# Performance work log

Measured on AMD Instinct MI355X. Metric: run time of the kernel, lower is better.

## Reference

```python
import jax, jax.numpy as jnp
import numpy as np

DIM = 768
N_HEADS = 12
HEAD_DIM = DIM // N_HEADS
BATCH = 2
SEQ = 4096


def setup_inputs() -> dict:
    key = jax.random.key(0)
    ks = jax.random.split(key, 9)
    s = 1.0 / np.sqrt(DIM)
    return {
        "x": jax.random.normal(ks[0], (BATCH, SEQ, DIM), dtype=jnp.float32),
        "Wq": jax.random.normal(ks[1], (DIM, DIM), dtype=jnp.float32) * s,
        "bq": jax.random.normal(ks[2], (DIM,), dtype=jnp.float32) * s,
        "Wk": jax.random.normal(ks[3], (DIM, DIM), dtype=jnp.float32) * s,
        "bk": jax.random.normal(ks[4], (DIM,), dtype=jnp.float32) * s,
        "Wv": jax.random.normal(ks[5], (DIM, DIM), dtype=jnp.float32) * s,
        "bv": jax.random.normal(ks[6], (DIM,), dtype=jnp.float32) * s,
        "Wo": jax.random.normal(ks[7], (DIM, DIM), dtype=jnp.float32) * s,
        "bo": jax.random.normal(ks[8], (DIM,), dtype=jnp.float32) * s,
    }


def reference(x, Wq, bq, Wk, bk, Wv, bv, Wo, bo):
    B, S, D = x.shape
    scale = 1.0 / np.sqrt(HEAD_DIM).astype(np.float32)
    # projections: [B,S,D] -> [B,H,S,Hd]
    def split_heads(t):
        return t.reshape(B, S, N_HEADS, HEAD_DIM).transpose(0, 2, 1, 3)
    q = split_heads(x @ Wq + bq)
    k = split_heads(x @ Wk + bk)
    v = split_heads(x @ Wv + bv)
    # full score matrix [B,H,S,S] as in the original (memory-bound)
    scores = jnp.einsum("bhqd,bhkd->bhqk", q, k) * scale
    attn = jax.nn.softmax(scores, axis=-1)
    out = jnp.einsum("bhqk,bhkd->bhqd", attn, v)
    out = out.transpose(0, 2, 1, 3).reshape(B, S, D)
    return out @ Wo + bo
```

## Files before the change

kernel.cpp:

```cpp
#include <hip/hip_runtime.h>
#include <hip/hip_bf16.h>
#include <math.h>

#define D_MODEL 768
#define NH 12
#define HD 64
#define BATCH 2
#define SEQ 4096
#define NROWS (BATCH * SEQ)

#define QSCALE 0.18033688011112042f

typedef __attribute__((ext_vector_type(8))) short short8;
typedef __attribute__((ext_vector_type(4))) short short4v;
typedef __attribute__((ext_vector_type(4))) float f32x4;
typedef __attribute__((ext_vector_type(16))) float f32x16;

__device__ inline unsigned short f2bf(float f) {
    __hip_bfloat16 h = __float2bfloat16(f);
    return *reinterpret_cast<unsigned short*>(&h);
}

__device__ __forceinline__ void async_ld16(const unsigned short* g, unsigned short* l) {
    __builtin_amdgcn_global_load_lds(
        (const __attribute__((address_space(1))) void*)g,
        (__attribute__((address_space(3))) void*)l, 16, 0, 0);
}

__global__ __launch_bounds__(256) void convert_x_k(
    const float* __restrict__ x, unsigned short* __restrict__ xb)
{
    size_t i = ((size_t)blockIdx.x * 256 + threadIdx.x) * 8;
    float4 a = *(const float4*)(x + i);
    float4 b = *(const float4*)(x + i + 4);
    short8 o;
    o[0] = (short)f2bf(a.x); o[1] = (short)f2bf(a.y);
    o[2] = (short)f2bf(a.z); o[3] = (short)f2bf(a.w);
    o[4] = (short)f2bf(b.x); o[5] = (short)f2bf(b.y);
    o[6] = (short)f2bf(b.z); o[7] = (short)f2bf(b.w);
    *(short8*)(xb + i) = o;
}

__global__ __launch_bounds__(256) void convert_wt_k(
    const float* __restrict__ Wq, const float* __restrict__ Wk,
    const float* __restrict__ Wv, const float* __restrict__ Wo,
    unsigned short* __restrict__ wt)
{
    const float* W = (blockIdx.z == 0) ? Wq : (blockIdx.z == 1) ? Wk
                   : (blockIdx.z == 2) ? Wv : Wo;
    unsigned short* dst = wt + (size_t)blockIdx.z * D_MODEL * D_MODEL;
    __shared__ float tile[64][65];
    const int k0 = blockIdx.x * 64, n0 = blockIdx.y * 64;
    const int t = threadIdx.x;
    const int r = t >> 2, seg = t & 3;
    const float* src = W + (size_t)(k0 + r) * D_MODEL + n0 + seg * 16;
    #pragma unroll
    for (int i = 0; i < 4; ++i) {
        float4 v = *(const float4*)(src + i * 4);
        tile[r][seg * 16 + i * 4 + 0] = v.x;
        tile[r][seg * 16 + i * 4 + 1] = v.y;
        tile[r][seg * 16 + i * 4 + 2] = v.z;
        tile[r][seg * 16 + i * 4 + 3] = v.w;
    }
    __syncthreads();
    unsigned short* d = dst + (size_t)(n0 + r) * D_MODEL + k0 + seg * 16;
    short8 o0, o1;
    #pragma unroll
    for (int j = 0; j < 8; ++j) o0[j] = (short)f2bf(tile[seg * 16 + j][r]);
    #pragma unroll
    for (int j = 0; j < 8; ++j) o1[j] = (short)f2bf(tile[seg * 16 + 8 + j][r]);
    *(short8*)(d) = o0;
    *(short8*)(d + 8) = o1;
}

__global__ __launch_bounds__(256) void qkv_mfma_k(
    const unsigned short* __restrict__ xb,
    const unsigned short* __restrict__ wt,
    const float* __restrict__ bq, const float* __restrict__ bk,
    const float* __restrict__ bv,
    unsigned short* __restrict__ qb,
    unsigned short* __restrict__ kb,
    unsigned short* __restrict__ vtb)
{
    __shared__ unsigned short As[128][64];
    __shared__ unsigned short Bs[64][64];
    const int z = blockIdx.z;
    const unsigned short* Wt = wt + (size_t)z * D_MODEL * D_MODEL;
    const float* bias = (z == 0) ? bq : (z == 1) ? bk : bv;
    const int t = threadIdx.x;
    const int w = t >> 6, lane = t & 63, quad = lane >> 4, col = lane & 15;
    const int r0 = blockIdx.x * 128;
    const int c0 = blockIdx.y * 64;

    f32x4 acc[2][4] = {};

    for (int kk = 0; kk < D_MODEL; kk += 64) {
        __syncthreads();
        #pragma unroll
        for (int j = 0; j < 4; ++j) {
            int c = (w * 4 + j) * 64 + lane;
            async_ld16(xb + (size_t)(r0 + (c >> 3)) * D_MODEL + kk + (c & 7) * 8,
                       &As[0][0] + (size_t)c * 8);
        }
        #pragma unroll
        for (int j = 0; j < 2; ++j) {
            int c = (w * 2 + j) * 64 + lane;
            async_ld16(Wt + (size_t)(c0 + (c >> 3)) * D_MODEL + kk + (c & 7) * 8,
                       &Bs[0][0] + (size_t)c * 8);
        }
        __syncthreads();
        #pragma unroll
        for (int ks = 0; ks < 2; ++ks) {
            short8 af[2], bf[4];
            af[0] = *(const short8*)&As[w * 32 + col][ks * 32 + quad * 8];
            af[1] = *(const short8*)&As[w * 32 + 16 + col][ks * 32 + quad * 8];
            #pragma unroll
            for (int nt = 0; nt < 4; ++nt)
                bf[nt] = *(const short8*)&Bs[nt * 16 + col][ks * 32 + quad * 8];
            #pragma unroll
            for (int mt = 0; mt < 2; ++mt)
                #pragma unroll
                for (int nt = 0; nt < 4; ++nt)
                    acc[mt][nt] = __builtin_amdgcn_mfma_f32_16x16x32_bf16(
                        af[mt], bf[nt], acc[mt][nt], 0, 0, 0);
        }
    }

    const int h = blockIdx.y;
    #pragma unroll
    for (int nt = 0; nt < 4; ++nt) {
        const float bv_ = bias[c0 + nt * 16 + col];
        const int hd = nt * 16 + col;
        #pragma unroll
        for (int mt = 0; mt < 2; ++mt) {
            #pragma unroll
            for (int reg = 0; reg < 4; ++reg) {
                int r = r0 + w * 32 + mt * 16 + quad * 4 + reg;
                int b = r >> 12, s = r & (SEQ - 1);
                float val = acc[mt][nt][reg] + bv_;
                size_t bh = (size_t)(b * NH + h);
                if (z == 0)
                    qb[(bh * SEQ + s) * HD + hd] = f2bf(val * QSCALE);
                else if (z == 1)
                    kb[(bh * SEQ + s) * HD + hd] = f2bf(val);
                else
                    vtb[(bh * HD + hd) * SEQ + s] = f2bf(val);
            }
        }
    }
}

__global__ __launch_bounds__(256) void out_mfma_k(
    const unsigned short* __restrict__ ab,
    const unsigned short* __restrict__ wot,
    const float* __restrict__ bo,
    float* __restrict__ out)
{
    __shared__ unsigned short As[128][64];
    __shared__ unsigned short Bs[64][64];
    const int t = threadIdx.x;
    const int w = t >> 6, lane = t & 63, quad = lane >> 4, col = lane & 15;
    const int r0 = blockIdx.x * 128;
    const int c0 = blockIdx.y * 64;

    f32x4 acc[2][4] = {};

    for (int kk = 0; kk < D_MODEL; kk += 64) {
        __syncthreads();
        #pragma unroll
        for (int j = 0; j < 4; ++j) {
            int c = (w * 4 + j) * 64 + lane;
            async_ld16(ab + (size_t)(r0 + (c >> 3)) * D_MODEL + kk + (c & 7) * 8,
                       &As[0][0] + (size_t)c * 8);
        }
        #pragma unroll
        for (int j = 0; j < 2; ++j) {
            int c = (w * 2 + j) * 64 + lane;
            async_ld16(wot + (size_t)(c0 + (c >> 3)) * D_MODEL + kk + (c & 7) * 8,
                       &Bs[0][0] + (size_t)c * 8);
        }
        __syncthreads();
        #pragma unroll
        for (int ks = 0; ks < 2; ++ks) {
            short8 af[2], bf[4];
            af[0] = *(const short8*)&As[w * 32 + col][ks * 32 + quad * 8];
            af[1] = *(const short8*)&As[w * 32 + 16 + col][ks * 32 + quad * 8];
            #pragma unroll
            for (int nt = 0; nt < 4; ++nt)
                bf[nt] = *(const short8*)&Bs[nt * 16 + col][ks * 32 + quad * 8];
            #pragma unroll
            for (int mt = 0; mt < 2; ++mt)
                #pragma unroll
                for (int nt = 0; nt < 4; ++nt)
                    acc[mt][nt] = __builtin_amdgcn_mfma_f32_16x16x32_bf16(
                        af[mt], bf[nt], acc[mt][nt], 0, 0, 0);
        }
    }

    #pragma unroll
    for (int nt = 0; nt < 4; ++nt) {
        const float bv_ = bo[c0 + nt * 16 + col];
        #pragma unroll
        for (int mt = 0; mt < 2; ++mt) {
            #pragma unroll
            for (int reg = 0; reg < 4; ++reg) {
                int r = r0 + w * 32 + mt * 16 + quad * 4 + reg;
                out[(size_t)r * D_MODEL + c0 + nt * 16 + col] = acc[mt][nt][reg] + bv_;
            }
        }
    }
}

__global__ __launch_bounds__(256) void flash_mfma_k(
    const unsigned short* __restrict__ qb,
    const unsigned short* __restrict__ kb,
    const unsigned short* __restrict__ vtb,
    unsigned short* __restrict__ ab)
{
    __shared__ unsigned short Ks[64][66];
    __shared__ unsigned short Vts[64][66];
    __shared__ unsigned short Ps[4][32][66];

    const int t = threadIdx.x;
    const int w = t >> 6, lane = t & 63;
    const int l31 = lane & 31, hi = lane >> 5;
    const int q0 = blockIdx.x * 128;
    const int h = blockIdx.y, b = blockIdx.z;
    const size_t bh = (size_t)b * NH + h;
    const unsigned short* qg = qb + bh * SEQ * HD;
    const unsigned short* kg = kb + bh * SEQ * HD;
    const unsigned short* vg = vtb + bh * HD * SEQ;

    short8 qf[4];
    {
        const unsigned short* src = qg + (size_t)(q0 + w * 32 + l31) * HD + hi * 8;
        #pragma unroll
        for (int ks = 0; ks < 4; ++ks)
            qf[ks] = *(const short8*)(src + ks * 16);
    }

    f32x16 oacc[2] = {};
    float lsum = 0.f;
    const int srow = lane, sseg = w;

    for (int kt = 0; kt < SEQ; kt += 64) {
        const unsigned short* kp = kg + (size_t)(kt + srow) * HD + sseg * 16;
        short8 kr0 = *(const short8*)(kp);
        short8 kr1 = *(const short8*)(kp + 8);
        const unsigned short* vp = vg + (size_t)srow * SEQ + kt + sseg * 16;
        short8 vr0 = *(const short8*)(vp);
        short8 vr1 = *(const short8*)(vp + 8);
        __syncthreads();
        *(short8*)&Ks[srow][sseg * 16]      = kr0;
        *(short8*)&Ks[srow][sseg * 16 + 8]  = kr1;
        *(short8*)&Vts[srow][sseg * 16]     = vr0;
        *(short8*)&Vts[srow][sseg * 16 + 8] = vr1;
        __syncthreads();

        #pragma unroll
        for (int kti = 0; kti < 2; ++kti) {
            f32x16 s = {};
            #pragma unroll
            for (int ks = 0; ks < 4; ++ks) {
                short8 kf = *(const short8*)&Ks[kti * 32 + l31][ks * 16 + hi * 8];
                s = __builtin_amdgcn_mfma_f32_32x32x16_bf16(kf, qf[ks], s, 0, 0, 0);
            }
            #pragma unroll
            for (int rq = 0; rq < 4; ++rq) {
                float p0 = __builtin_amdgcn_exp2f(s[rq * 4 + 0]);
                float p1 = __builtin_amdgcn_exp2f(s[rq * 4 + 1]);
                float p2 = __builtin_amdgcn_exp2f(s[rq * 4 + 2]);
                float p3 = __builtin_amdgcn_exp2f(s[rq * 4 + 3]);
                lsum += (p0 + p1) + (p2 + p3);
                short4v pk;
                pk[0] = (short)f2bf(p0);
                pk[1] = (short)f2bf(p1);
                pk[2] = (short)f2bf(p2);
                pk[3] = (short)f2bf(p3);
                *(short4v*)&Ps[w][l31][kti * 32 + rq * 8 + hi * 4] = pk;
            }
        }

        #pragma unroll
        for (int ks = 0; ks < 4; ++ks) {
            short8 pf = *(const short8*)&Ps[w][l31][ks * 16 + hi * 8];
            #pragma unroll
            for (int dt = 0; dt < 2; ++dt) {
                short8 vf = *(const short8*)&Vts[dt * 32 + l31][ks * 16 + hi * 8];
                oacc[dt] = __builtin_amdgcn_mfma_f32_32x32x16_bf16(
                    vf, pf, oacc[dt], 0, 0, 0);
            }
        }
    }

    lsum += __shfl_xor(lsum, 32);
    float inv = 1.0f / lsum;
    int s = q0 + w * 32 + l31;
    unsigned short* dst = ab + ((size_t)b * SEQ + s) * D_MODEL + h * HD;
    #pragma unroll
    for (int dt = 0; dt < 2; ++dt) {
        #pragma unroll
        for (int rq = 0; rq < 4; ++rq) {
            short4v o4;
            o4[0] = (short)f2bf(oacc[dt][rq * 4 + 0] * inv);
            o4[1] = (short)f2bf(oacc[dt][rq * 4 + 1] * inv);
            o4[2] = (short)f2bf(oacc[dt][rq * 4 + 2] * inv);
            o4[3] = (short)f2bf(oacc[dt][rq * 4 + 3] * inv);
            *(short4v*)(dst + dt * 32 + rq * 8 + hi * 4) = o4;
        }
    }
}

extern "C" void kernel_launch(void* const* d_in, const int* in_sizes, int n_in,
                              void* d_out, int out_size, void* d_ws, size_t ws_size,
                              hipStream_t stream)
{
    const float* x  = (const float*)d_in[0];
    const float* Wq = (const float*)d_in[1];
    const float* bq = (const float*)d_in[2];
    const float* Wk = (const float*)d_in[3];
    const float* bk = (const float*)d_in[4];
    const float* Wv = (const float*)d_in[5];
    const float* bv = (const float*)d_in[6];
    const float* Wo = (const float*)d_in[7];
    const float* bo = (const float*)d_in[8];
    float* out = (float*)d_out;

    const size_t n_x  = (size_t)NROWS * D_MODEL;
    const size_t n_w  = (size_t)D_MODEL * D_MODEL;
    unsigned short* xb  = (unsigned short*)d_ws;
    unsigned short* wt  = xb + n_x;
    unsigned short* qb  = wt + 4 * n_w;
    unsigned short* kb  = qb + n_x;
    unsigned short* vtb = kb + n_x;
    unsigned short* ab  = vtb + n_x;
    const size_t need = ((size_t)4 * n_x + 4 * n_w + n_x) * sizeof(unsigned short);
    if (ws_size < need) return;

    convert_x_k<<<dim3((int)(n_x / 2048)), 256, 0, stream>>>(x, xb);
    convert_wt_k<<<dim3(12, 12, 4), 256, 0, stream>>>(Wq, Wk, Wv, Wo, wt);
    qkv_mfma_k<<<dim3(NROWS / 128, D_MODEL / 64, 3), 256, 0, stream>>>(
        xb, wt, bq, bk, bv, qb, kb, vtb);
    flash_mfma_k<<<dim3(SEQ / 128, NH, BATCH), 256, 0, stream>>>(qb, kb, vtb, ab);
    out_mfma_k<<<dim3(NROWS / 128, D_MODEL / 64), 256, 0, stream>>>(
        ab, wt + 3 * n_w, bo, out);
}
```

Baseline: 320.2 us.

## Split key tile across warp pairs with 2x2 register blocking and LDS reduction

Reorganizes the flash attention block so each pair of warps shares 64 queries and each warp handles half of every 64-key tile. Each warp loads its K fragments once and reuses them across two query tiles, and reuses each V fragment across two query tiles. The goal is to cut LDS reads per MFMA. The cost is a cross-warp reduction of partial output accumulators and row sums through shared memory at the end, plus more accumulator registers, which may lower occupancy.

Result: slower. 697.7 us (+117.9%).

```diff
diff --git a/kernel.cpp b/kernel.cpp
--- a/kernel.cpp
+++ b/kernel.cpp
@@ -217,13 +217,17 @@
     const unsigned short* __restrict__ vtb,
     unsigned short* __restrict__ ab)
 {
-    __shared__ unsigned short Ks[64][66];
-    __shared__ unsigned short Vts[64][66];
-    __shared__ unsigned short Ps[4][32][66];
+    __shared__ __align__(16) unsigned char smem[34304];
+    unsigned short (*Ks)[66]  = (unsigned short(*)[66])smem;
+    unsigned short (*Vts)[66] = (unsigned short(*)[66])(smem + 8448);
+    unsigned short (*Ps)[34]  = (unsigned short(*)[34])(smem + 16896);
+    float* Red = (float*)smem;
 
     const int t = threadIdx.x;
     const int w = t >> 6, lane = t & 63;
     const int l31 = lane & 31, hi = lane >> 5;
+    const int qgrp = w >> 1;
+    const int khalf = w & 1;
     const int q0 = blockIdx.x * 128;
     const int h = blockIdx.y, b = blockIdx.z;
     const size_t bh = (size_t)b * NH + h;
@@ -231,16 +235,18 @@
     const unsigned short* kg = kb + bh * SEQ * HD;
     const unsigned short* vg = vtb + bh * HD * SEQ;
 
-    short8 qf[4];
-    {
-        const unsigned short* src = qg + (size_t)(q0 + w * 32 + l31) * HD + hi * 8;
-        #pragma unroll
-        for (int ks = 0; ks < 4; ++ks)
-            qf[ks] = *(const short8*)(src + ks * 16);
-    }
-
-    f32x16 oacc[2] = {};
-    float lsum = 0.f;
+    short8 qf[2][4];
+    #pragma unroll
+    for (int qt = 0; qt < 2; ++qt) {
+        const unsigned short* src =
+            qg + (size_t)(q0 + qgrp * 64 + qt * 32 + l31) * HD + hi * 8;
+        #pragma unroll
+        for (int ks2 = 0; ks2 < 4; ++ks2)
+            qf[qt][ks2] = *(const short8*)(src + ks2 * 16);
+    }
+
+    f32x16 oacc[2][2] = {};
+    float lsum[2] = {0.f, 0.f};
     const int srow = lane, sseg = w;
 
     for (int kt = 0; kt < SEQ; kt += 64) {
@@ -257,56 +263,97 @@
         *(short8*)&Vts[srow][sseg * 16 + 8] = vr1;
         __syncthreads();
 
-        #pragma unroll
-        for (int kti = 0; kti < 2; ++kti) {
-            f32x16 s = {};
-            #pragma unroll
-            for (int ks = 0; ks < 4; ++ks) {
-                short8 kf = *(const short8*)&Ks[kti * 32 + l31][ks * 16 + hi * 8];
-                s = __builtin_amdgcn_mfma_f32_32x32x16_bf16(kf, qf[ks], s, 0, 0, 0);
-            }
-            #pragma unroll
-            for (int rq = 0; rq < 4; ++rq) {
-                float p0 = __builtin_amdgcn_exp2f(s[rq * 4 + 0]);
-                float p1 = __builtin_amdgcn_exp2f(s[rq * 4 + 1]);
-                float p2 = __builtin_amdgcn_exp2f(s[rq * 4 + 2]);
-                float p3 = __builtin_amdgcn_exp2f(s[rq * 4 + 3]);
-                lsum += (p0 + p1) + (p2 + p3);
-                short4v pk;
-                pk[0] = (short)f2bf(p0);
-                pk[1] = (short)f2bf(p1);
-                pk[2] = (short)f2bf(p2);
-                pk[3] = (short)f2bf(p3);
-                *(short4v*)&Ps[w][l31][kti * 32 + rq * 8 + hi * 4] = pk;
-            }
-        }
-
-        #pragma unroll
-        for (int ks = 0; ks < 4; ++ks) {
-            short8 pf = *(const short8*)&Ps[w][l31][ks * 16 + hi * 8];
+        {
+            short8 kf[4];
+            #pragma unroll
+            for (int ks2 = 0; ks2 < 4; ++ks2)
+                kf[ks2] = *(const short8*)&Ks[khalf * 32 + l31][ks2 * 16 + hi * 8];
+            #pragma unroll
+            for (int qt = 0; qt < 2; ++qt) {
+                f32x16 s = {};
+                #pragma unroll
+                for (int ks2 = 0; ks2 < 4; ++ks2)
+                    s = __builtin_amdgcn_mfma_f32_32x32x16_bf16(
+                        kf[ks2], qf[qt][ks2], s, 0, 0, 0);
+                #pragma unroll
+                for (int rq = 0; rq < 4; ++rq) {
+                    float p0 = __builtin_amdgcn_exp2f(s[rq * 4 + 0]);
+                    float p1 = __builtin_amdgcn_exp2f(s[rq * 4 + 1]);
+                    float p2 = __builtin_amdgcn_exp2f(s[rq * 4 + 2]);
+                    float p3 = __builtin_amdgcn_exp2f(s[rq * 4 + 3]);
+                    lsum[qt] += (p0 + p1) + (p2 + p3);
+                    short4v pk;
+                    pk[0] = (short)f2bf(p0);
+                    pk[1] = (short)f2bf(p1);
+                    pk[2] = (short)f2bf(p2);
+                    pk[3] = (short)f2bf(p3);
+                    *(short4v*)&Ps[w * 64 + qt * 32 + l31][rq * 8 + hi * 4] = pk;
+                }
+            }
+        }
+
+        #pragma unroll
+        for (int ks = 0; ks < 2; ++ks) {
+            short8 pf[2];
+            #pragma unroll
+            for (int qt = 0; qt < 2; ++qt)
+                pf[qt] = *(const short8*)&Ps[w * 64 + qt * 32 + l31][ks * 16 + hi * 8];
             #pragma unroll
             for (int dt = 0; dt < 2; ++dt) {
-                short8 vf = *(const short8*)&Vts[dt * 32 + l31][ks * 16 + hi * 8];
-                oacc[dt] = __builtin_amdgcn_mfma_f32_32x32x16_bf16(
-                    vf, pf, oacc[dt], 0, 0, 0);
-            }
-        }
-    }
-
-    lsum += __shfl_xor(lsum, 32);
-    float inv = 1.0f / lsum;
-    int s = q0 + w * 32 + l31;
-    unsigned short* dst = ab + ((size_t)b * SEQ + s) * D_MODEL + h * HD;
-    #pragma unroll
-    for (int dt = 0; dt < 2; ++dt) {
-        #pragma unroll
-        for (int rq = 0; rq < 4; ++rq) {
-            short4v o4;
-            o4[0] = (short)f2bf(oacc[dt][rq * 4 + 0] * inv);
-            o4[1] = (short)f2bf(oacc[dt][rq * 4 + 1] * inv);
-            o4[2] = (short)f2bf(oacc[dt][rq * 4 + 2] * inv);
-            o4[3] = (short)f2bf(oacc[dt][rq * 4 + 3] * inv);
-            *(short4v*)(dst + dt * 32 + rq * 8 + hi * 4) = o4;
+                short8 vf = *(const short8*)
+                    &Vts[dt * 32 + l31][khalf * 32 + ks * 16 + hi * 8];
+                #pragma unroll
+                for (int qt = 0; qt < 2; ++qt)
+                    oacc[dt][qt] = __builtin_amdgcn_mfma_f32_32x32x16_bf16(
+                        vf, pf[qt], oacc[dt][qt], 0, 0, 0);
+            }
+        }
+    }
+
+    lsum[0] += __shfl_xor(lsum[0], 32);
+    lsum[1] += __shfl_xor(lsum[1], 32);
+
+    __syncthreads();
+    if (khalf == 1) {
+        float* R = Red + qgrp * (64 * 66) + lane * 66;
+        #pragma unroll
+        for (int dt = 0; dt < 2; ++dt)
+            #pragma unroll
+            for (int qt = 0; qt < 2; ++qt)
+                #pragma unroll
+                for (int reg = 0; reg < 16; ++reg)
+                    R[dt * 32 + qt * 16 + reg] = oacc[dt][qt][reg];
+        R[64] = lsum[0];
+        R[65] = lsum[1];
+    }
+    __syncthreads();
+    if (khalf == 0) {
+        const float* R = Red + qgrp * (64 * 66) + lane * 66;
+        #pragma unroll
+        for (int dt = 0; dt < 2; ++dt)
+            #pragma unroll
+            for (int qt = 0; qt < 2; ++qt)
+                #pragma unroll
+                for (int reg = 0; reg < 16; ++reg)
+                    oacc[dt][qt][reg] += R[dt * 32 + qt * 16 + reg];
+        float ltot[2] = {lsum[0] + R[64], lsum[1] + R[65]};
+        #pragma unroll
+        for (int qt = 0; qt < 2; ++qt) {
+            float inv = 1.0f / ltot[qt];
+            int s = q0 + qgrp * 64 + qt * 32 + l31;
+            unsigned short* dst = ab + ((size_t)b * SEQ + s) * D_MODEL + h * HD;
+            #pragma unroll
+            for (int dt = 0; dt < 2; ++dt) {
+                #pragma unroll
+                for (int rq = 0; rq < 4; ++rq) {
+                    short4v o4;
+                    o4[0] = (short)f2bf(oacc[dt][qt][rq * 4 + 0] * inv);
+                    o4[1] = (short)f2bf(oacc[dt][qt][rq * 4 + 1] * inv);
+                    o4[2] = (short)f2bf(oacc[dt][qt][rq * 4 + 2] * inv);
+                    o4[3] = (short)f2bf(oacc[dt][qt][rq * 4 + 3] * inv);
+                    *(short4v*)(dst + dt * 32 + rq * 8 + hi * 4) = o4;
+                }
+            }
         }
     }
 }
```
